# Kernel tuning notes

Hardware: AMD Instinct MI355X
Metric: run time of the kernel (lower is better)

Reference implementation:

```python
import jax, jax.numpy as jnp
import numpy as np

B, S, D = 64, 1024, 256
N_HEADS = 1
HEAD_DIM = D // N_HEADS
MASK_VAL = -10000.0


def setup_inputs() -> dict:
    key = jax.random.key(0)
    k1, k2, k3 = jax.random.split(key, 3)
    x = jax.random.normal(k1, (B, S, D), dtype=jnp.float32)
    W_qkv = jax.random.normal(k2, (D, 3 * D), dtype=jnp.float32) * 0.02
    b_qkv = jnp.zeros((3 * D,), dtype=jnp.float32)
    W_out = jax.random.normal(k3, (D, D), dtype=jnp.float32) * 0.02
    b_out = jnp.zeros((D,), dtype=jnp.float32)
    return {"x": x, "W_qkv": W_qkv, "b_qkv": b_qkv, "W_out": W_out, "b_out": b_out}


def reference(x, W_qkv, b_qkv, W_out, b_out):
    # QKV projection: [B,S,3D]
    qkv = jnp.einsum('bsd,df->bsf', x, W_qkv) + b_qkv
    q, k, v = jnp.split(qkv, 3, axis=2)
    # split heads -> [B,H,S,hd] (H=1)
    def split_heads(t):
        return t.reshape(B, S, N_HEADS, HEAD_DIM).transpose(0, 2, 1, 3)
    q, k, v = split_heads(q), split_heads(k), split_heads(v)
    # scaled scores [B,H,S,S]
    scores = jnp.einsum('bhqd,bhkd->bhqk', q, k) / jnp.sqrt(jnp.float32(HEAD_DIM))
    causal = jnp.tril(jnp.ones((1, 1, S, S), dtype=bool))
    scores = jnp.where(causal, scores, jnp.float32(MASK_VAL))
    attn = jax.nn.softmax(scores, axis=-1)  # dropout deterministic (training=False)
    out = jnp.einsum('bhqk,bhkd->bhqd', attn, v)
    # merge heads -> [B,S,D]
    out = out.transpose(0, 2, 1, 3).reshape(B, S, D)
    out = jnp.einsum('bsd,de->bse', out, W_out) + b_out
    return out, attn
```

## Files before the change

### kernel.cpp

```cpp
#include <hip/hip_runtime.h>
#include <hip/hip_bf16.h>

#define BB 64
#define SS 1024
#define DDIM 256

typedef unsigned short u16;
typedef __attribute__((ext_vector_type(4))) float f4;
typedef __attribute__((ext_vector_type(8))) short bf16x8;
typedef __attribute__((ext_vector_type(4))) short bf16x4;
typedef __attribute__((ext_vector_type(4))) float f32x4;

__device__ inline u16 f2b(float f) {
  unsigned int u = __float_as_uint(f);
  unsigned int r = (u + 0x7fffu + ((u >> 16) & 1u)) >> 16;
  return (u16)r;
}

#define GLOAD16(g, l)                                                  \
  __builtin_amdgcn_global_load_lds(                                    \
      (const __attribute__((address_space(1))) void*)(g),              \
      (__attribute__((address_space(3))) void*)(l), 16, 0, 0)

__global__ __launch_bounds__(256) void cast_x(const float* __restrict__ x,
                                              u16* __restrict__ xb, int n8) {
  int i = blockIdx.x * 256 + threadIdx.x;
  const int stride = gridDim.x * 256;
  for (; i < n8; i += stride) {
    f4 a = ((const f4*)x)[2 * i];
    f4 b = ((const f4*)x)[2 * i + 1];
    bf16x8 o;
    o[0] = f2b(a[0]); o[1] = f2b(a[1]); o[2] = f2b(a[2]); o[3] = f2b(a[3]);
    o[4] = f2b(b[0]); o[5] = f2b(b[1]); o[6] = f2b(b[2]); o[7] = f2b(b[3]);
    ((bf16x8*)xb)[i] = o;
  }
}

__global__ __launch_bounds__(256) void cast_w(const float* __restrict__ Wqkv,
                                              const float* __restrict__ Wout,
                                              u16* __restrict__ Wqkvt,
                                              u16* __restrict__ Woutt) {
  int t = blockIdx.x * 256 + threadIdx.x;
  if (t < 256 * 768) {
    int k = t / 768, n = t % 768;
    Wqkvt[n * 256 + k] = f2b(Wqkv[t]);
  }
  if (t < 256 * 256) {
    int k = t / 256, n = t % 256;
    Woutt[n * 256 + k] = f2b(Wout[t]);
  }
}

template <int EPI, int NXT>
__global__ __launch_bounds__(512) void gemm_mfma(
    const u16* __restrict__ A, const u16* __restrict__ Bt,
    const float* __restrict__ bias, float* __restrict__ outF,
    u16* __restrict__ Qb, u16* __restrict__ Kb, u16* __restrict__ Vt) {
  __shared__ u16 As[128 * 64];
  __shared__ u16 Bs[256 * 64];
  const int t = threadIdx.x;
  const int w = t >> 6, l = t & 63;
  const int lr = l & 15, lg = l >> 4;
  const int id = blockIdx.x;
  const int r8 = id & 7;
  const int tt = id >> 3;
  const int xt = tt % NXT;
  const int yt = (tt / NXT) * 8 + r8;
  const int m0 = yt * 128, n0 = xt * 256;
  const int wm = (w >> 2) * 64, wn = (w & 3) * 64;

  f32x4 acc[4][4] = {};

  for (int k0 = 0; k0 < 256; k0 += 64) {
    __syncthreads();
#pragma unroll
    for (int j = 0; j < 2; ++j) {
      const int idx = t + j * 512;
      const int row = idx >> 3, c = idx & 7;
      f4 va = *(const f4*)&A[(size_t)(m0 + row) * 256 + k0 + c * 8];
      *(f4*)&As[row * 64 + ((c ^ (row & 7)) * 8)] = va;
    }
#pragma unroll
    for (int j = 0; j < 4; ++j) {
      const int idx = t + j * 512;
      const int row = idx >> 3, c = idx & 7;
      f4 vb = *(const f4*)&Bt[(size_t)(n0 + row) * 256 + k0 + c * 8];
      *(f4*)&Bs[row * 64 + ((c ^ (row & 7)) * 8)] = vb;
    }
    __syncthreads();
#pragma unroll
    for (int kc = 0; kc < 2; ++kc) {
      bf16x8 af[4], bfr[4];
#pragma unroll
      for (int f = 0; f < 4; ++f) {
        int ar = wm + f * 16 + lr;
        af[f] = *(const bf16x8*)&As[ar * 64 + (((kc * 4 + lg) ^ (ar & 7)) * 8)];
        int br = wn + f * 16 + lr;
        bfr[f] = *(const bf16x8*)&Bs[br * 64 + (((kc * 4 + lg) ^ (br & 7)) * 8)];
      }
#pragma unroll
      for (int i = 0; i < 4; ++i)
#pragma unroll
        for (int jn = 0; jn < 4; ++jn)
          acc[i][jn] = __builtin_amdgcn_mfma_f32_16x16x32_bf16(
              af[i], bfr[jn], acc[i][jn], 0, 0, 0);
    }
  }

#pragma unroll
  for (int i = 0; i < 4; ++i) {
    const int mbase = m0 + wm + i * 16 + lg * 4;
#pragma unroll
    for (int jn = 0; jn < 4; ++jn) {
      const int n = n0 + wn + jn * 16 + lr;
      const float bv = bias[n];
      if (EPI == 0) {
#pragma unroll
        for (int r = 0; r < 4; ++r)
          outF[(size_t)(mbase + r) * 256 + n] = acc[i][jn][r] + bv;
      } else {
        if (n < 256) {
#pragma unroll
          for (int r = 0; r < 4; ++r)
            Qb[(size_t)(mbase + r) * 256 + n] = f2b(acc[i][jn][r] + bv);
        } else if (n < 512) {
#pragma unroll
          for (int r = 0; r < 4; ++r)
            Kb[(size_t)(mbase + r) * 256 + (n - 256)] = f2b(acc[i][jn][r] + bv);
        } else {
          const int d = n - 512;
          const int b = mbase >> 10, sl = mbase & 1023;
          bf16x4 pk;
#pragma unroll
          for (int r = 0; r < 4; ++r) pk[r] = f2b(acc[i][jn][r] + bv);
          *(bf16x4*)&Vt[((size_t)b * 256 + d) * 1024 + sl] = pk;
        }
      }
    }
  }
}

__global__ __launch_bounds__(256) void attn_fused(
    const u16* __restrict__ Qg, const u16* __restrict__ Kg,
    const u16* __restrict__ Vtg, float* __restrict__ attn,
    u16* __restrict__ outa) {
  __shared__ u16 pool[35328];
  u16* Ks = pool;
  u16* Vs = pool + 16384;
  u16* Ps = pool + 32768;

  const int t = threadIdx.x;
  const int w = t >> 6, l = t & 63;
  const int lr = l & 15, lg = l >> 4;
  const int id = blockIdx.x;
  const int b = (id & 7) * 8 + ((id >> 3) & 7);
  const int pair = id >> 6;
  const int qta = pair, qtb = 15 - pair;
  const int d0w = w * 64;

  const u16* Kbase = Kg + (size_t)b * SS * DDIM;
  const u16* Vbase = Vtg + (size_t)b * DDIM * SS;

  auto stageK64 = [&](int kt, int buf) {
#pragma unroll
    for (int i = 0; i < 8; ++i) {
      const int rr = 16 * w + 2 * i + (l >> 5);
      const int chunk = l & 31;
      const int csrc = (chunk & 24) | ((chunk & 7) ^ (rr & 7));
      const u16* g = Kbase + (size_t)(kt * 64 + rr) * DDIM + csrc * 8;
      GLOAD16(g, pool + buf * 16384 + (16 * w + 2 * i) * 256);
    }
  };
  auto stageK = [&](int kt, int buf) {
    const int rbase = 8 * w;
#pragma unroll
    for (int i = 0; i < 4; ++i) {
      const int rr = rbase + 2 * i + (l >> 5);
      const int chunk = l & 31;
      const int csrc = (chunk & 24) | ((chunk & 7) ^ (rr & 7));
      const u16* g = Kbase + (size_t)(kt * 32 + rr) * DDIM + csrc * 8;
      GLOAD16(g, Ks + buf * 8192 + (rbase + 2 * i) * 256);
    }
  };
  auto stageV = [&](int kt, int buf) {
    const int dbase = 64 * w;
#pragma unroll
    for (int i = 0; i < 4; ++i) {
      const int dd = dbase + 16 * i + (l >> 2);
      const u16* g = Vbase + (size_t)dd * SS + kt * 32 + (l & 3) * 8;
      GLOAD16(g, Vs + buf * 8192 + (dbase + 16 * i) * 32);
    }
  };
  auto loadQ = [&](int qt, bf16x8* qf) {
    const u16* qb = Qg + ((size_t)(b * SS + qt * 64 + w * 16 + lr)) * DDIM;
#pragma unroll
    for (int kc = 0; kc < 8; ++kc)
      qf[kc] = *(const bf16x8*)&qb[kc * 32 + lg * 8];
  };

  bf16x8 qfA[8], qfB[8];
  loadQ(qta, qfA);
  loadQ(qtb, qfB);
  float raA[4] = {0.f, 0.f, 0.f, 0.f}, raB[4] = {0.f, 0.f, 0.f, 0.f};

  stageK64(0, 0);
  __syncthreads();
  for (int kt = 0; kt <= qtb; ++kt) {
    const int buf = kt & 1;
    if (kt < qtb) stageK64(kt + 1, buf ^ 1);
    const bool doA = (kt <= qta);
#pragma unroll
    for (int sf = 0; sf < 4; ++sf) {
      const int srow = sf * 16 + lr;
      const u16* kr = pool + buf * 16384 + srow * 256;
      f32x4 sA = {0.f, 0.f, 0.f, 0.f}, sB = {0.f, 0.f, 0.f, 0.f};
#pragma unroll
      for (int kc = 0; kc < 8; ++kc) {
        const int c = kc * 4 + lg;
        const int ch = (c & 24) | ((c & 7) ^ (srow & 7));
        bf16x8 bfr = *(const bf16x8*)&kr[ch * 8];
        sB = __builtin_amdgcn_mfma_f32_16x16x32_bf16(qfB[kc], bfr, sB, 0, 0, 0);
        if (doA)
          sA = __builtin_amdgcn_mfma_f32_16x16x32_bf16(qfA[kc], bfr, sA, 0, 0, 0);
      }
      const int scol = kt * 64 + sf * 16 + lr;
      {
        const int qrow = qtb * 64 + w * 16 + lg * 4;
#pragma unroll
        for (int r = 0; r < 4; ++r)
          raB[r] += (scol <= qrow + r) ? __expf(sB[r] * 0.0625f) : 0.f;
      }
      if (doA) {
        const int qrow = qta * 64 + w * 16 + lg * 4;
#pragma unroll
        for (int r = 0; r < 4; ++r)
          raA[r] += (scol <= qrow + r) ? __expf(sA[r] * 0.0625f) : 0.f;
      }
    }
    __syncthreads();
  }
#pragma unroll
  for (int m = 1; m < 16; m <<= 1) {
#pragma unroll
    for (int r = 0; r < 4; ++r) {
      raA[r] += __shfl_xor(raA[r], m, 64);
      raB[r] += __shfl_xor(raB[r], m, 64);
    }
  }
  float invA[4], invB[4];
#pragma unroll
  for (int r = 0; r < 4; ++r) {
    invA[r] = 1.0f / raA[r];
    invB[r] = 1.0f / raB[r];
  }

  for (int tile = 0; tile < 2; ++tile) {
    const int qt = tile ? qtb : qta;
    const int last = 2 * qt + 1;
    bf16x8 qf[8];
    loadQ(qt, qf);
    float inv[4];
#pragma unroll
    for (int r = 0; r < 4; ++r) inv[r] = tile ? invB[r] : invA[r];
    f32x4 oacc[4][4];
#pragma unroll
    for (int qb = 0; qb < 4; ++qb)
#pragma unroll
      for (int df = 0; df < 4; ++df) oacc[qb][df] = (f32x4){0.f, 0.f, 0.f, 0.f};

    float* attnw = attn + ((size_t)(b * SS + qt * 64 + w * 16)) * SS;

    __syncthreads();
    stageK(0, 0);
    stageV(0, 0);
    __syncthreads();

    for (int kt = 0; kt <= last; ++kt) {
      const int buf = kt & 1;
#pragma unroll
      for (int sf = 0; sf < 2; ++sf) {
        const int srow = sf * 16 + lr;
        const u16* kr = Ks + buf * 8192 + srow * 256;
        f32x4 s = {0.f, 0.f, 0.f, 0.f};
#pragma unroll
        for (int kc = 0; kc < 8; ++kc) {
          const int c = kc * 4 + lg;
          const int ch = (c & 24) | ((c & 7) ^ (srow & 7));
          bf16x8 bfr = *(const bf16x8*)&kr[ch * 8];
          s = __builtin_amdgcn_mfma_f32_16x16x32_bf16(qf[kc], bfr, s, 0, 0, 0);
        }
        const int scol = kt * 32 + sf * 16 + lr;
        const int qrow = qt * 64 + w * 16 + lg * 4;
#pragma unroll
        for (int r = 0; r < 4; ++r) {
          const float e = (scol <= qrow + r) ? __expf(s[r] * 0.0625f) : 0.f;
          Ps[(w * 16 + lg * 4 + r) * 40 + sf * 16 + lr] = f2b(e * inv[r]);
        }
      }
#pragma unroll
      for (int g2 = 0; g2 < 2; ++g2) {
        const int row = g2 * 8 + (l >> 3);
        const int col = (l & 7) * 4;
        bf16x4 pv = *(const bf16x4*)&Ps[(w * 16 + row) * 40 + col];
        f4 o;
#pragma unroll
        for (int j = 0; j < 4; ++j)
          o[j] = __uint_as_float(((unsigned)(u16)pv[j]) << 16);
        *(f4*)&attnw[(size_t)row * SS + kt * 32 + col] = o;
      }
      __syncthreads();
      if (kt < last) {
        stageK(kt + 1, buf ^ 1);
        stageV(kt + 1, buf ^ 1);
      }
      bf16x8 vfr[4];
      const u16* vb = Vs + buf * 8192;
#pragma unroll
      for (int df = 0; df < 4; ++df)
        vfr[df] = *(const bf16x8*)&vb[(d0w + df * 16 + lr) * 32 + lg * 8];
#pragma unroll
      for (int qb = 0; qb < 4; ++qb) {
        bf16x8 pa = *(const bf16x8*)&Ps[(qb * 16 + lr) * 40 + lg * 8];
#pragma unroll
        for (int df = 0; df < 4; ++df)
          oacc[qb][df] = __builtin_amdgcn_mfma_f32_16x16x32_bf16(
              pa, vfr[df], oacc[qb][df], 0, 0, 0);
      }
      __syncthreads();
    }

    {
      const f4 z = {0.f, 0.f, 0.f, 0.f};
      for (int c0 = (qt + 1) * 64; c0 < SS; c0 += 32) {
#pragma unroll
        for (int g2 = 0; g2 < 2; ++g2) {
          const int row = g2 * 8 + (l >> 3);
          *(f4*)&attnw[(size_t)row * SS + c0 + (l & 7) * 4] = z;
        }
      }
    }

#pragma unroll
    for (int qb = 0; qb < 4; ++qb)
#pragma unroll
      for (int df = 0; df < 4; ++df)
#pragma unroll
        for (int r = 0; r < 4; ++r)
          pool[(qb * 16 + lg * 4 + r) * 264 + d0w + df * 16 + lr] =
              f2b(oacc[qb][df][r]);
    __syncthreads();
    {
      const size_t obase = (size_t)(b * SS + qt * 64);
#pragma unroll
      for (int i = 0; i < 8; ++i) {
        const int row = w * 16 + 2 * i + (l >> 5);
        bf16x8 v = *(const bf16x8*)&pool[row * 264 + (l & 31) * 8];
        *(bf16x8*)&outa[(obase + row) * DDIM + (l & 31) * 8] = v;
      }
    }
  }
}

extern "C" void kernel_launch(void* const* d_in, const int* in_sizes, int n_in,
                              void* d_out, int out_size, void* d_ws,
                              size_t ws_size, hipStream_t stream) {
  const float* x    = (const float*)d_in[0];
  const float* Wqkv = (const float*)d_in[1];
  const float* bqkv = (const float*)d_in[2];
  const float* Wout = (const float*)d_in[3];
  const float* bout = (const float*)d_in[4];

  float* out  = (float*)d_out;
  float* attn = out + (size_t)BB * SS * DDIM;

  const size_t NTOK = (size_t)BB * SS;
  u16* ws = (u16*)d_ws;
  u16* xb    = ws;
  u16* Qb    = xb + NTOK * DDIM;
  u16* Kb    = Qb + NTOK * DDIM;
  u16* Vt    = Kb + NTOK * DDIM;
  u16* outa  = Vt + NTOK * DDIM;
  u16* Wqkvt = outa + NTOK * DDIM;
  u16* Woutt = Wqkvt + 768 * 256;

  cast_x<<<2048, 256, 0, stream>>>(x, xb, (int)(NTOK * DDIM / 8));
  cast_w<<<768, 256, 0, stream>>>(Wqkv, Wout, Wqkvt, Woutt);

  gemm_mfma<1, 3><<<1536, 512, 0, stream>>>(xb, Wqkvt, bqkv, nullptr, Qb, Kb,
                                            Vt);
  attn_fused<<<512, 256, 0, stream>>>(Qb, Kb, Vt, attn, outa);
  gemm_mfma<0, 1><<<512, 512, 0, stream>>>(outa, Woutt, bout, out, nullptr,
                                           nullptr, nullptr);
}
```

Measured before the change: 255.0 us.

## Single-pass attention: keep unnormalized probabilities in LDS, normalize at write-out

The two-pass attention kernel computed row sums in a first pass and then recomputed QK^T in a second pass. It is replaced by a single pass over 32-row query tiles. Unnormalized exp scores for the whole causal row are kept in a large swizzled LDS buffer, row sums are reduced across waves, and both the attn output and PV accumulators are normalized at the end. K and V prefetch moves from global_load_lds double buffering to register prefetch, and the grid grows from 512 to 2048 blocks. This removes the duplicated QK^T compute and exp work. In exchange it uses more LDS per block, P is rounded to bf16 before normalization, and each iteration now has more syncs.

```diff
diff --git a/kernel.cpp b/kernel.cpp
--- a/kernel.cpp
+++ b/kernel.cpp
@@ -6,6 +6,7 @@
 #define DDIM 256
 
 typedef unsigned short u16;
+typedef unsigned int u32;
 typedef __attribute__((ext_vector_type(4))) float f4;
 typedef __attribute__((ext_vector_type(8))) short bf16x8;
 typedef __attribute__((ext_vector_type(4))) short bf16x4;
@@ -16,11 +17,9 @@
   unsigned int r = (u + 0x7fffu + ((u >> 16) & 1u)) >> 16;
   return (u16)r;
 }
-
-#define GLOAD16(g, l)                                                  \
-  __builtin_amdgcn_global_load_lds(                                    \
-      (const __attribute__((address_space(1))) void*)(g),              \
-      (__attribute__((address_space(3))) void*)(l), 16, 0, 0)
+__device__ inline float b2f(u16 v) {
+  return __uint_as_float(((u32)v) << 16);
+}
 
 __global__ __launch_bounds__(256) void cast_x(const float* __restrict__ x,
                                               u16* __restrict__ xb, int n8) {
@@ -144,219 +143,190 @@
     const u16* __restrict__ Qg, const u16* __restrict__ Kg,
     const u16* __restrict__ Vtg, float* __restrict__ attn,
     u16* __restrict__ outa) {
-  __shared__ u16 pool[35328];
-  u16* Ks = pool;
-  u16* Vs = pool + 16384;
-  u16* Ps = pool + 32768;
+  __shared__ u16 pool[40960];
+  u16* P = pool;
+  u16* Ks = pool + 32768;
+  float* rsF = (float*)(pool + 32768);
 
   const int t = threadIdx.x;
   const int w = t >> 6, l = t & 63;
   const int lr = l & 15, lg = l >> 4;
   const int id = blockIdx.x;
-  const int b = (id & 7) * 8 + ((id >> 3) & 7);
-  const int pair = id >> 6;
-  const int qta = pair, qtb = 15 - pair;
-  const int d0w = w * 64;
+  const int b = 8 * (id & 7) + ((id >> 3) & 7);
+  const int zb = id >> 6;
+  const int qt = 15 - (zb >> 1);
+  const int h = 1 - (zb & 1);
+  const int qrow0 = qt * 64 + h * 32;
+  const int last = 2 * qt + h;
+  const int qh = w & 1, sfh = w >> 1;
+  const int d0 = w * 64;
 
   const u16* Kbase = Kg + (size_t)b * SS * DDIM;
   const u16* Vbase = Vtg + (size_t)b * DDIM * SS;
 
-  auto stageK64 = [&](int kt, int buf) {
-#pragma unroll
-    for (int i = 0; i < 8; ++i) {
-      const int rr = 16 * w + 2 * i + (l >> 5);
-      const int chunk = l & 31;
-      const int csrc = (chunk & 24) | ((chunk & 7) ^ (rr & 7));
-      const u16* g = Kbase + (size_t)(kt * 64 + rr) * DDIM + csrc * 8;
-      GLOAD16(g, pool + buf * 16384 + (16 * w + 2 * i) * 256);
-    }
-  };
-  auto stageK = [&](int kt, int buf) {
-    const int rbase = 8 * w;
-#pragma unroll
-    for (int i = 0; i < 4; ++i) {
-      const int rr = rbase + 2 * i + (l >> 5);
-      const int chunk = l & 31;
-      const int csrc = (chunk & 24) | ((chunk & 7) ^ (rr & 7));
-      const u16* g = Kbase + (size_t)(kt * 32 + rr) * DDIM + csrc * 8;
-      GLOAD16(g, Ks + buf * 8192 + (rbase + 2 * i) * 256);
-    }
-  };
-  auto stageV = [&](int kt, int buf) {
-    const int dbase = 64 * w;
-#pragma unroll
-    for (int i = 0; i < 4; ++i) {
-      const int dd = dbase + 16 * i + (l >> 2);
-      const u16* g = Vbase + (size_t)dd * SS + kt * 32 + (l & 3) * 8;
-      GLOAD16(g, Vs + buf * 8192 + (dbase + 16 * i) * 32);
-    }
-  };
-  auto loadQ = [&](int qt, bf16x8* qf) {
-    const u16* qb = Qg + ((size_t)(b * SS + qt * 64 + w * 16 + lr)) * DDIM;
+  bf16x8 qf[8];
+  {
+    const u16* qp = Qg + ((size_t)(b * SS + qrow0 + qh * 16 + lr)) * DDIM;
 #pragma unroll
     for (int kc = 0; kc < 8; ++kc)
-      qf[kc] = *(const bf16x8*)&qb[kc * 32 + lg * 8];
-  };
-
-  bf16x8 qfA[8], qfB[8];
-  loadQ(qta, qfA);
-  loadQ(qtb, qfB);
-  float raA[4] = {0.f, 0.f, 0.f, 0.f}, raB[4] = {0.f, 0.f, 0.f, 0.f};
-
-  stageK64(0, 0);
+      qf[kc] = *(const bf16x8*)&qp[kc * 32 + lg * 8];
+  }
+
+  {
+    f4 kreg[4];
+#pragma unroll
+    for (int j = 0; j < 4; ++j) {
+      const int cid = t + j * 256;
+      const int row = cid >> 5, ch = cid & 31;
+      kreg[j] = *(const f4*)&Kbase[(size_t)row * 256 + ch * 8];
+#pragma unroll
+      for (int jj = 0; jj <= 0; ++jj) {
+        const int sw = (ch & 24) | ((ch & 7) ^ (row & 7));
+        *(f4*)&Ks[row * 256 + sw * 8] = kreg[j];
+      }
+    }
+  }
   __syncthreads();
-  for (int kt = 0; kt <= qtb; ++kt) {
-    const int buf = kt & 1;
-    if (kt < qtb) stageK64(kt + 1, buf ^ 1);
-    const bool doA = (kt <= qta);
-#pragma unroll
-    for (int sf = 0; sf < 4; ++sf) {
-      const int srow = sf * 16 + lr;
-      const u16* kr = pool + buf * 16384 + srow * 256;
-      f32x4 sA = {0.f, 0.f, 0.f, 0.f}, sB = {0.f, 0.f, 0.f, 0.f};
+
+  bf16x8 vfr[4];
+#pragma unroll
+  for (int df = 0; df < 4; ++df)
+    vfr[df] = *(const bf16x8*)&Vbase[(size_t)(d0 + df * 16 + lr) * SS + lg * 8];
+
+  float ra[4] = {0.f, 0.f, 0.f, 0.f};
+  f32x4 oacc[2][4];
+#pragma unroll
+  for (int qb = 0; qb < 2; ++qb)
+#pragma unroll
+    for (int df = 0; df < 4; ++df) oacc[qb][df] = (f32x4){0.f, 0.f, 0.f, 0.f};
+
+  for (int kt = 0; kt <= last; ++kt) {
+    f4 kregN[4];
+    bf16x8 vfrN[4];
+    if (kt < last) {
+#pragma unroll
+      for (int j = 0; j < 4; ++j) {
+        const int cid = t + j * 256;
+        const int row = cid >> 5, ch = cid & 31;
+        kregN[j] =
+            *(const f4*)&Kbase[(size_t)((kt + 1) * 32 + row) * 256 + ch * 8];
+      }
+#pragma unroll
+      for (int df = 0; df < 4; ++df)
+        vfrN[df] = *(const bf16x8*)&Vbase[(size_t)(d0 + df * 16 + lr) * SS +
+                                          (kt + 1) * 32 + lg * 8];
+    }
+    {
+      const int srow = sfh * 16 + lr;
+      f32x4 s = {0.f, 0.f, 0.f, 0.f};
 #pragma unroll
       for (int kc = 0; kc < 8; ++kc) {
         const int c = kc * 4 + lg;
         const int ch = (c & 24) | ((c & 7) ^ (srow & 7));
-        bf16x8 bfr = *(const bf16x8*)&kr[ch * 8];
-        sB = __builtin_amdgcn_mfma_f32_16x16x32_bf16(qfB[kc], bfr, sB, 0, 0, 0);
-        if (doA)
-          sA = __builtin_amdgcn_mfma_f32_16x16x32_bf16(qfA[kc], bfr, sA, 0, 0, 0);
-      }
-      const int scol = kt * 64 + sf * 16 + lr;
-      {
-        const int qrow = qtb * 64 + w * 16 + lg * 4;
+        bf16x8 bfr = *(const bf16x8*)&Ks[srow * 256 + ch * 8];
+        s = __builtin_amdgcn_mfma_f32_16x16x32_bf16(qf[kc], bfr, s, 0, 0, 0);
+      }
+      const int qmin = qrow0 + qh * 16;
+      float p[4];
+      if (kt * 32 + sfh * 16 + 16 <= qmin) {
+#pragma unroll
+        for (int r = 0; r < 4; ++r) p[r] = __expf(s[r] * 0.0625f);
+      } else {
+        const int scol = kt * 32 + sfh * 16 + lr;
 #pragma unroll
         for (int r = 0; r < 4; ++r)
-          raB[r] += (scol <= qrow + r) ? __expf(sB[r] * 0.0625f) : 0.f;
-      }
-      if (doA) {
-        const int qrow = qta * 64 + w * 16 + lg * 4;
-#pragma unroll
-        for (int r = 0; r < 4; ++r)
-          raA[r] += (scol <= qrow + r) ? __expf(sA[r] * 0.0625f) : 0.f;
+          p[r] = (scol <= qmin + lg * 4 + r) ? __expf(s[r] * 0.0625f) : 0.f;
+      }
+#pragma unroll
+      for (int r = 0; r < 4; ++r) {
+        ra[r] += p[r];
+        const int row = qh * 16 + lg * 4 + r;
+        const int col = kt * 32 + sfh * 16 + lr;
+        const int c = col >> 3;
+        const int sw = (c & ~7) | ((c & 7) ^ (row & 7));
+        P[row * 1024 + sw * 8 + (col & 7)] = f2b(p[r]);
       }
     }
     __syncthreads();
-  }
-#pragma unroll
-  for (int m = 1; m < 16; m <<= 1) {
+    if (kt < last) {
+#pragma unroll
+      for (int j = 0; j < 4; ++j) {
+        const int cid = t + j * 256;
+        const int row = cid >> 5, ch = cid & 31;
+        const int sw = (ch & 24) | ((ch & 7) ^ (row & 7));
+        *(f4*)&Ks[row * 256 + sw * 8] = kregN[j];
+      }
+    }
+#pragma unroll
+    for (int qb = 0; qb < 2; ++qb) {
+      const int row = qb * 16 + lr;
+      const int c = kt * 4 + lg;
+      const int sw = (c & ~7) | ((c & 7) ^ (row & 7));
+      bf16x8 pa = *(const bf16x8*)&P[row * 1024 + sw * 8];
+#pragma unroll
+      for (int df = 0; df < 4; ++df)
+        oacc[qb][df] = __builtin_amdgcn_mfma_f32_16x16x32_bf16(
+            pa, vfr[df], oacc[qb][df], 0, 0, 0);
+    }
+    if (kt < last) {
+#pragma unroll
+      for (int df = 0; df < 4; ++df) vfr[df] = vfrN[df];
+      __syncthreads();
+    }
+  }
+
+#pragma unroll
+  for (int m = 1; m < 16; m <<= 1)
+#pragma unroll
+    for (int r = 0; r < 4; ++r) ra[r] += __shfl_xor(ra[r], m, 64);
+  if (lr == 0) {
+#pragma unroll
+    for (int r = 0; r < 4; ++r)
+      rsF[sfh * 32 + qh * 16 + lg * 4 + r] = ra[r];
+  }
+  __syncthreads();
+
+  {
+    float* attnb = attn + ((size_t)(b * SS + qrow0)) * SS;
+    const int row = w * 8 + (l >> 3);
+    const float invr = 1.0f / (rsF[row] + rsF[32 + row]);
+    const int kend = (last + 1) * 32;
+    for (int c0 = 0; c0 < kend; c0 += 32) {
+      const int col = c0 + (l & 7) * 4;
+      const int c = col >> 3;
+      const int sw = (c & ~7) | ((c & 7) ^ (row & 7));
+      bf16x4 pv = *(const bf16x4*)&P[row * 1024 + sw * 8 + (col & 7)];
+      f4 o;
+#pragma unroll
+      for (int j = 0; j < 4; ++j) o[j] = b2f((u16)pv[j]) * invr;
+      *(f4*)&attnb[(size_t)row * SS + col] = o;
+    }
+    const f4 z = {0.f, 0.f, 0.f, 0.f};
+    for (int c0 = kend; c0 < SS; c0 += 32)
+      *(f4*)&attnb[(size_t)row * SS + c0 + (l & 7) * 4] = z;
+  }
+  __syncthreads();
+
+#pragma unroll
+  for (int qb = 0; qb < 2; ++qb) {
 #pragma unroll
     for (int r = 0; r < 4; ++r) {
-      raA[r] += __shfl_xor(raA[r], m, 64);
-      raB[r] += __shfl_xor(raB[r], m, 64);
-    }
-  }
-  float invA[4], invB[4];
-#pragma unroll
-  for (int r = 0; r < 4; ++r) {
-    invA[r] = 1.0f / raA[r];
-    invB[r] = 1.0f / raB[r];
-  }
-
-  for (int tile = 0; tile < 2; ++tile) {
-    const int qt = tile ? qtb : qta;
-    const int last = 2 * qt + 1;
-    bf16x8 qf[8];
-    loadQ(qt, qf);
-    float inv[4];
-#pragma unroll
-    for (int r = 0; r < 4; ++r) inv[r] = tile ? invB[r] : invA[r];
-    f32x4 oacc[4][4];
-#pragma unroll
-    for (int qb = 0; qb < 4; ++qb)
-#pragma unroll
-      for (int df = 0; df < 4; ++df) oacc[qb][df] = (f32x4){0.f, 0.f, 0.f, 0.f};
-
-    float* attnw = attn + ((size_t)(b * SS + qt * 64 + w * 16)) * SS;
-
-    __syncthreads();
-    stageK(0, 0);
-    stageV(0, 0);
-    __syncthreads();
-
-    for (int kt = 0; kt <= last; ++kt) {
-      const int buf = kt & 1;
-#pragma unroll
-      for (int sf = 0; sf < 2; ++sf) {
-        const int srow = sf * 16 + lr;
-        const u16* kr = Ks + buf * 8192 + srow * 256;
-        f32x4 s = {0.f, 0.f, 0.f, 0.f};
-#pragma unroll
-        for (int kc = 0; kc < 8; ++kc) {
-          const int c = kc * 4 + lg;
-          const int ch = (c & 24) | ((c & 7) ^ (srow & 7));
-          bf16x8 bfr = *(const bf16x8*)&kr[ch * 8];
-          s = __builtin_amdgcn_mfma_f32_16x16x32_bf16(qf[kc], bfr, s, 0, 0, 0);
-        }
-        const int scol = kt * 32 + sf * 16 + lr;
-        const int qrow = qt * 64 + w * 16 + lg * 4;
-#pragma unroll
-        for (int r = 0; r < 4; ++r) {
-          const float e = (scol <= qrow + r) ? __expf(s[r] * 0.0625f) : 0.f;
-          Ps[(w * 16 + lg * 4 + r) * 40 + sf * 16 + lr] = f2b(e * inv[r]);
-        }
-      }
-#pragma unroll
-      for (int g2 = 0; g2 < 2; ++g2) {
-        const int row = g2 * 8 + (l >> 3);
-        const int col = (l & 7) * 4;
-        bf16x4 pv = *(const bf16x4*)&Ps[(w * 16 + row) * 40 + col];
-        f4 o;
-#pragma unroll
-        for (int j = 0; j < 4; ++j)
-          o[j] = __uint_as_float(((unsigned)(u16)pv[j]) << 16);
-        *(f4*)&attnw[(size_t)row * SS + kt * 32 + col] = o;
-      }
-      __syncthreads();
-      if (kt < last) {
-        stageK(kt + 1, buf ^ 1);
-        stageV(kt + 1, buf ^ 1);
-      }
-      bf16x8 vfr[4];
-      const u16* vb = Vs + buf * 8192;
+      const int row = qb * 16 + lg * 4 + r;
+      const float invv = 1.0f / (rsF[row] + rsF[32 + row]);
 #pragma unroll
       for (int df = 0; df < 4; ++df)
-        vfr[df] = *(const bf16x8*)&vb[(d0w + df * 16 + lr) * 32 + lg * 8];
-#pragma unroll
-      for (int qb = 0; qb < 4; ++qb) {
-        bf16x8 pa = *(const bf16x8*)&Ps[(qb * 16 + lr) * 40 + lg * 8];
-#pragma unroll
-        for (int df = 0; df < 4; ++df)
-          oacc[qb][df] = __builtin_amdgcn_mfma_f32_16x16x32_bf16(
-              pa, vfr[df], oacc[qb][df], 0, 0, 0);
-      }
-      __syncthreads();
-    }
-
-    {
-      const f4 z = {0.f, 0.f, 0.f, 0.f};
-      for (int c0 = (qt + 1) * 64; c0 < SS; c0 += 32) {
-#pragma unroll
-        for (int g2 = 0; g2 < 2; ++g2) {
-          const int row = g2 * 8 + (l >> 3);
-          *(f4*)&attnw[(size_t)row * SS + c0 + (l & 7) * 4] = z;
-        }
-      }
-    }
-
-#pragma unroll
-    for (int qb = 0; qb < 4; ++qb)
-#pragma unroll
-      for (int df = 0; df < 4; ++df)
-#pragma unroll
-        for (int r = 0; r < 4; ++r)
-          pool[(qb * 16 + lg * 4 + r) * 264 + d0w + df * 16 + lr] =
-              f2b(oacc[qb][df][r]);
-    __syncthreads();
-    {
-      const size_t obase = (size_t)(b * SS + qt * 64);
-#pragma unroll
-      for (int i = 0; i < 8; ++i) {
-        const int row = w * 16 + 2 * i + (l >> 5);
-        bf16x8 v = *(const bf16x8*)&pool[row * 264 + (l & 31) * 8];
-        *(bf16x8*)&outa[(obase + row) * DDIM + (l & 31) * 8] = v;
-      }
+        pool[row * 264 + d0 + df * 16 + lr] = f2b(oacc[qb][df][r] * invv);
+    }
+  }
+  __syncthreads();
+  {
+    const int row = t >> 3;
+    const int cb = (t & 7) * 32;
+    u16* og = outa + ((size_t)(b * SS + qrow0 + row)) * DDIM + cb;
+#pragma unroll
+    for (int k = 0; k < 4; ++k) {
+      bf16x8 v = *(const bf16x8*)&pool[row * 264 + cb + k * 8];
+      *(bf16x8*)&og[k * 8] = v;
     }
   }
 }
@@ -388,7 +358,7 @@
 
   gemm_mfma<1, 3><<<1536, 512, 0, stream>>>(xb, Wqkvt, bqkv, nullptr, Qb, Kb,
                                             Vt);
-  attn_fused<<<512, 256, 0, stream>>>(Qb, Kb, Vt, attn, outa);
+  attn_fused<<<2048, 256, 0, stream>>>(Qb, Kb, Vt, attn, outa);
   gemm_mfma<0, 1><<<512, 512, 0, stream>>>(outa, Woutt, bout, out, nullptr,
                                            nullptr, nullptr);
 }
```

Measured after the change: 249.6 us (median of 2 runs). -2.1%, faster.
